# Kernel tuning notes

Hardware: AMD Instinct MI355X
Metric: run time of the kernel (lower is better)

The kernel has to match this reference:

```python
import jax, jax.numpy as jnp
import numpy as np

D_MODEL = 1024
N_HEADS = 16
FEATURE_DIM = 16
HEAD_DIM = D_MODEL // N_HEADS  # 64
EPS = 1e-12


def taylor_exp(x):
    """2nd-order Taylor feature map of exp(q^T k / sqrt(d)).
    x: (b, h, l, d) -> (b, h, l, 1 + d + d^2)"""
    d = x.shape[-1]
    rd = jnp.sqrt(jnp.asarray(d, x.dtype))      # sqrt(d)
    rrd = jnp.sqrt(rd)                          # d^(1/4)
    r2 = jnp.sqrt(jnp.asarray(2.0, x.dtype))
    x2 = (x[..., :, None] * x[..., None, :]).reshape(*x.shape[:-1], d * d) / r2
    ones = jnp.ones_like(x[..., :1])
    return jnp.concatenate([ones, x / rrd, x2 / rd], axis=-1)


def setup_inputs() -> dict:
    key = jax.random.key(0)
    k0, k1, k2, k3, k4 = jax.random.split(key, 5)
    b, l = 1, 1024
    scale = 1.0 / np.sqrt(D_MODEL)
    hidden_states = jax.random.normal(k0, (b, l, D_MODEL), dtype=jnp.float32)
    Wq = jax.random.normal(k1, (N_HEADS * FEATURE_DIM, D_MODEL), dtype=jnp.float32) * scale
    Wk = jax.random.normal(k2, (N_HEADS * FEATURE_DIM, D_MODEL), dtype=jnp.float32) * scale
    Wv = jax.random.normal(k3, (N_HEADS * HEAD_DIM, D_MODEL), dtype=jnp.float32) * scale
    Wo = jax.random.normal(k4, (D_MODEL, N_HEADS * HEAD_DIM), dtype=jnp.float32) * scale
    return {"hidden_states": hidden_states, "Wq": Wq, "Wk": Wk, "Wv": Wv, "Wo": Wo}


def reference(hidden_states, Wq, Wk, Wv, Wo):
    b, l, _ = hidden_states.shape
    # projections (bias-free)
    q = (hidden_states @ Wq.T).reshape(b, l, N_HEADS, FEATURE_DIM).transpose(0, 2, 1, 3)
    k = (hidden_states @ Wk.T).reshape(b, l, N_HEADS, FEATURE_DIM).transpose(0, 2, 1, 3)
    v = (hidden_states @ Wv.T).reshape(b, l, N_HEADS, HEAD_DIM).transpose(0, 2, 1, 3)
    qf = taylor_exp(q)   # (b, h, l, D) with D = 1 + d + d^2 = 273
    kf = taylor_exp(k)
    # causal linear attention via associative KV accumulation
    # kv_state[l] = sum_{t<=l} phi(k_t) outer v_t  -> (b, h, l, head_dim, D)
    kv_state = jnp.cumsum(kf[..., None, :] * v[..., :, None], axis=2)
    num = jnp.einsum('bhlD,bhldD->bhld', qf, kv_state)
    den = jnp.einsum('bhlD,bhlD->bhl', qf, jnp.cumsum(kf, axis=2))[..., None] + EPS
    y = num / den                                # (b, h, l, head_dim)
    y = y.transpose(0, 2, 1, 3).reshape(b, l, N_HEADS * HEAD_DIM)
    return y @ Wo.T
```

## Files before the change

### kernel.cpp

```cpp
#include <hip/hip_runtime.h>

#define LSEQ 1024
#define DMODEL 1024
#define NHEADS 16
#define FDIM 16
#define HDIM 64
#define CHUNK 64
#define NCHUNK 16
#define NSPLIT 4

typedef __attribute__((ext_vector_type(8))) short short8;
typedef __attribute__((ext_vector_type(4))) float floatx4;

__device__ __forceinline__ unsigned short f2bf(float f) {
    return __builtin_bit_cast(unsigned short, (__bf16)f);
}

__device__ __forceinline__ int block_detect_fp32(const unsigned short* wq) {
    __shared__ int cnt;
    if (threadIdx.x == 0) cnt = 0;
    __syncthreads();
    int bad = 0;
    for (int i = threadIdx.x; i < 1024; i += blockDim.x) {
        int e = (wq[i] >> 7) & 0xFF;
        if (e >= 143 || (e > 0 && e <= 80)) bad++;
    }
    if (bad) atomicAdd(&cnt, bad);
    __syncthreads();
    return cnt > 128;
}

#define U_QB   0
#define U_KB   262144
#define U_VT   524288
#define U_YB   1572864
#define U_END  2621440

#define MFMA(a, b, c) __builtin_amdgcn_mfma_f32_16x16x32_bf16((a), (b), (c), 0, 0, 0)

__device__ __forceinline__ void gemm64_body(
    unsigned short (&As)[64][136], unsigned short (&Bs)[64][136],
    const void* Araw, int a_fp32, int arow0,
    const void* Braw, int b_fp32, int brow0, floatx4 acc[4]) {
    int t = threadIdx.x;
    int r = t >> 2, c0 = (t & 3) * 32;
    int wave = t >> 6, lane = t & 63;
    int ml = lane & 15, q4 = lane >> 4;
    int mq = (wave >> 1) * 32, nq = (wave & 1) * 32;
    #pragma unroll
    for (int i = 0; i < 4; ++i) acc[i] = (floatx4){0.f, 0.f, 0.f, 0.f};

    short8 av[4], bv[4], av2[4], bv2[4];
    auto cvt8 = [](float4 f0, float4 f1) {
        short8 x;
        x[0] = (short)f2bf(f0.x); x[1] = (short)f2bf(f0.y);
        x[2] = (short)f2bf(f0.z); x[3] = (short)f2bf(f0.w);
        x[4] = (short)f2bf(f1.x); x[5] = (short)f2bf(f1.y);
        x[6] = (short)f2bf(f1.z); x[7] = (short)f2bf(f1.w);
        return x;
    };
    auto stage = [&](int k0, short8* a, short8* b) {
        if (!a_fp32) {
            const unsigned short* Ap = (const unsigned short*)Araw + (size_t)(arow0 + r) * DMODEL + k0 + c0;
            #pragma unroll
            for (int j = 0; j < 4; ++j) a[j] = *(const short8*)(Ap + j * 8);
        } else {
            const float* Ap = (const float*)Araw + (size_t)(arow0 + r) * DMODEL + k0 + c0;
            #pragma unroll
            for (int j = 0; j < 4; ++j)
                a[j] = cvt8(*(const float4*)(Ap + j * 8), *(const float4*)(Ap + j * 8 + 4));
        }
        if (!b_fp32) {
            const unsigned short* Bp = (const unsigned short*)Braw + (size_t)(brow0 + r) * DMODEL + k0 + c0;
            #pragma unroll
            for (int j = 0; j < 4; ++j) b[j] = *(const short8*)(Bp + j * 8);
        } else {
            const float* Bp = (const float*)Braw + (size_t)(brow0 + r) * DMODEL + k0 + c0;
            #pragma unroll
            for (int j = 0; j < 4; ++j)
                b[j] = cvt8(*(const float4*)(Bp + j * 8), *(const float4*)(Bp + j * 8 + 4));
        }
    };

    stage(0, av, bv);
    for (int k0 = 0; k0 < DMODEL; k0 += 128) {
        __syncthreads();
        #pragma unroll
        for (int j = 0; j < 4; ++j) {
            *(short8*)&As[r][c0 + j * 8] = av[j];
            *(short8*)&Bs[r][c0 + j * 8] = bv[j];
        }
        __syncthreads();
        if (k0 + 128 < DMODEL) stage(k0 + 128, av2, bv2);
        #pragma unroll
        for (int kk = 0; kk < 4; ++kk) {
            short8 a0 = *(const short8*)&As[mq + ml][kk * 32 + q4 * 8];
            short8 a1 = *(const short8*)&As[mq + 16 + ml][kk * 32 + q4 * 8];
            short8 b0 = *(const short8*)&Bs[nq + ml][kk * 32 + q4 * 8];
            short8 b1 = *(const short8*)&Bs[nq + 16 + ml][kk * 32 + q4 * 8];
            acc[0] = MFMA(a0, b0, acc[0]); acc[1] = MFMA(a0, b1, acc[1]);
            acc[2] = MFMA(a1, b0, acc[2]); acc[3] = MFMA(a1, b1, acc[3]);
        }
        #pragma unroll
        for (int j = 0; j < 4; ++j) { av[j] = av2[j]; bv[j] = bv2[j]; }
    }
}

__global__ __launch_bounds__(256) void qkv_gemm(
    const void* __restrict__ hidR, const void* __restrict__ WqR,
    const void* __restrict__ WkR, const void* __restrict__ WvR,
    unsigned short* __restrict__ qb, unsigned short* __restrict__ kb,
    unsigned short* __restrict__ vt) {
    int fp32 = block_detect_fp32((const unsigned short*)WqR);
    __shared__ __align__(16) unsigned short As[64][136];
    __shared__ __align__(16) unsigned short Bs[64][136];
    int nb = blockIdx.x, mb = blockIdx.y;
    const void* Braw; unsigned short* Cout; int ldc, col0, br0, isv;
    if (nb < 4)      { Braw = WqR; br0 = nb * 64;       Cout = qb; ldc = 256;  col0 = nb * 64;       isv = 0; }
    else if (nb < 8) { Braw = WkR; br0 = (nb - 4) * 64; Cout = kb; ldc = 256;  col0 = (nb - 4) * 64; isv = 0; }
    else             { Braw = WvR; br0 = (nb - 8) * 64; Cout = vt; ldc = 0;    col0 = (nb - 8) * 64; isv = 1; }

    floatx4 acc[4];
    gemm64_body(As, Bs, hidR, fp32, mb * 64, Braw, fp32, br0, acc);

    int wave = threadIdx.x >> 6, lane = threadIdx.x & 63;
    int ml = lane & 15, q4 = lane >> 4;
    int mq = (wave >> 1) * 32, nq = (wave & 1) * 32;
    if (!isv) {
        #pragma unroll
        for (int mi = 0; mi < 2; ++mi)
            #pragma unroll
            for (int ni = 0; ni < 2; ++ni) {
                floatx4 a = acc[mi * 2 + ni];
                int nloc = nq + ni * 16 + ml;
                #pragma unroll
                for (int r4 = 0; r4 < 4; ++r4) {
                    int row = mb * 64 + mq + mi * 16 + q4 * 4 + r4;
                    Cout[(size_t)row * ldc + col0 + nloc] = f2bf(a[r4]);
                }
            }
    } else {
        #pragma unroll
        for (int mi = 0; mi < 2; ++mi)
            #pragma unroll
            for (int ni = 0; ni < 2; ++ni) {
                floatx4 a = acc[mi * 2 + ni];
                int n = col0 + nq + ni * 16 + ml;
                int row0 = mb * 64 + mq + mi * 16 + q4 * 4;
                ushort4 o;
                o.x = f2bf(a[0]); o.y = f2bf(a[1]);
                o.z = f2bf(a[2]); o.w = f2bf(a[3]);
                *(ushort4*)&vt[(size_t)n * 1024 + row0] = o;
            }
    }
}

__global__ __launch_bounds__(256) void flash_partial(
    const unsigned short* __restrict__ qb, const unsigned short* __restrict__ kb,
    const unsigned short* __restrict__ vt,
    float* __restrict__ numW, float* __restrict__ denW) {
    int idx = blockIdx.x & 255;
    int s = blockIdx.x >> 8;
    int h = idx & 15, c = idx >> 4;
    int n = c + 1;
    int j0 = (n * s) >> 2;
    int j1 = ((n * (s + 1)) >> 2) - 1;
    int l0 = c * CHUNK;
    __shared__ __align__(16) unsigned short qs[64][40];
    __shared__ __align__(16) unsigned short ksm[64][40];
    __shared__ __align__(16) unsigned short vT[80][72];
    __shared__ __align__(16) unsigned short P[64][72];
    int t = threadIdx.x, lane = t & 63, wave = t >> 6;
    int ml = lane & 15, q4 = lane >> 4;
    int m0 = wave * 16;
    int sm = t >> 2, si4 = (t & 3) * 4, sc16 = (t & 3) * 16;

    {
        *(ushort4*)&qs[sm][si4] = *(const ushort4*)&qb[(size_t)(l0 + sm) * 256 + h * 16 + si4];
        ushort4 z = {0, 0, 0, 0};
        *(ushort4*)&qs[sm][16 + si4]  = z;
        *(ushort4*)&ksm[sm][16 + si4] = z;
    }
    if (t < 64) {
        vT[64][t] = 0x3F80;
        #pragma unroll
        for (int i = 65; i < 80; ++i) vT[i][t] = 0;
    }

    auto load_kv = [&](int j, ushort4& kr, short8& v0, short8& v1) {
        kr = *(const ushort4*)&kb[(size_t)(j * 64 + sm) * 256 + h * 16 + si4];
        const unsigned short* vp = vt + (size_t)(h * 64 + sm) * 1024 + j * 64 + sc16;
        v0 = *(const short8*)vp;
        v1 = *(const short8*)(vp + 8);
    };

    floatx4 acc[5];
    #pragma unroll
    for (int i = 0; i < 5; ++i) acc[i] = (floatx4){0.f, 0.f, 0.f, 0.f};

    ushort4 kr, kr2; short8 va, vb2, va2, vb22;
    if (j0 <= j1) {
        load_kv(j0, kr, va, vb2);
        for (int j = j0; j <= j1; ++j) {
            *(ushort4*)&ksm[sm][si4] = kr;
            *(short8*)&vT[sm][sc16]     = va;
            *(short8*)&vT[sm][sc16 + 8] = vb2;
            __syncthreads();
            if (j < j1) load_kv(j + 1, kr2, va2, vb22);

            short8 aq = *(const short8*)&qs[m0 + ml][q4 * 8];
            bool diag = (j == c);
            int qloc = m0 + ml;
            #pragma unroll
            for (int nt = 0; nt < 4; ++nt) {
                short8 bk = *(const short8*)&ksm[nt * 16 + ml][q4 * 8];
                floatx4 s4 = {0.f, 0.f, 0.f, 0.f};
                s4 = MFMA(bk, aq, s4);
                ushort4 pw;
                #pragma unroll
                for (int r = 0; r < 4; ++r) {
                    int tloc = nt * 16 + q4 * 4 + r;
                    float sc = s4[r];
                    float p = 1.f + 0.25f * sc + 0.03125f * sc * sc;
                    if (diag && tloc > qloc) p = 0.f;
                    ((unsigned short*)&pw)[r] = f2bf(p);
                }
                *(ushort4*)&P[qloc][nt * 16 + q4 * 4] = pw;
            }

            #pragma unroll
            for (int k0 = 0; k0 < 64; k0 += 32) {
                short8 ap = *(const short8*)&P[m0 + ml][k0 + q4 * 8];
                #pragma unroll
                for (int nt = 0; nt < 5; ++nt) {
                    short8 av = *(const short8*)&vT[nt * 16 + ml][k0 + q4 * 8];
                    acc[nt] = MFMA(av, ap, acc[nt]);
                }
            }
            __syncthreads();
            kr = kr2; va = va2; vb2 = vb22;
        }
    }

    float* np = numW + ((size_t)idx * NSPLIT + s) * 4096 + (m0 + ml) * 64;
    #pragma unroll
    for (int nt = 0; nt < 4; ++nt)
        *(floatx4*)&np[nt * 16 + q4 * 4] = acc[nt];
    if (lane < 16) denW[((size_t)idx * NSPLIT + s) * 64 + m0 + lane] = acc[4][0];
}

__global__ __launch_bounds__(256) void attn_combine(
    const float* __restrict__ numW, const float* __restrict__ denW,
    unsigned short* __restrict__ ybB) {
    int idx = blockIdx.x;
    int h = idx & 15, c = idx >> 4;
    int l0 = c * CHUNK;
    int t = threadIdx.x;
    int row = t >> 2, col0 = (t & 3) * 16;
    const float* nb_ = numW + (size_t)idx * NSPLIT * 4096 + row * 64 + col0;
    const float* db_ = denW + (size_t)idx * NSPLIT * 64 + row;
    float den = db_[0] + db_[64] + db_[128] + db_[192] + 1e-12f;
    float dinv = 1.f / den;
    float sum[16];
    #pragma unroll
    for (int u = 0; u < 16; u += 4) {
        float4 a0 = *(const float4*)(nb_ + u);
        float4 a1 = *(const float4*)(nb_ + 4096 + u);
        float4 a2 = *(const float4*)(nb_ + 8192 + u);
        float4 a3 = *(const float4*)(nb_ + 12288 + u);
        sum[u + 0] = a0.x + a1.x + a2.x + a3.x;
        sum[u + 1] = a0.y + a1.y + a2.y + a3.y;
        sum[u + 2] = a0.z + a1.z + a2.z + a3.z;
        sum[u + 3] = a0.w + a1.w + a2.w + a3.w;
    }
    short8 o0, o1;
    #pragma unroll
    for (int u = 0; u < 8; ++u)  o0[u] = (short)f2bf(sum[u] * dinv);
    #pragma unroll
    for (int u = 0; u < 8; ++u)  o1[u] = (short)f2bf(sum[u + 8] * dinv);
    unsigned short* yp = ybB + (size_t)(l0 + row) * 1024 + h * 64 + col0;
    *(short8*)yp       = o0;
    *(short8*)(yp + 8) = o1;
}

__global__ __launch_bounds__(256) void out_gemm(
    const unsigned short* __restrict__ A, const void* __restrict__ WoR,
    void* __restrict__ outv, const unsigned short* __restrict__ wqraw) {
    int fp32 = block_detect_fp32(wqraw);
    __shared__ __align__(16) unsigned short As[64][136];
    __shared__ __align__(16) unsigned short Bs[64][136];
    int nb = blockIdx.x, mb = blockIdx.y;

    floatx4 acc[4];
    gemm64_body(As, Bs, A, 0, mb * 64, WoR, fp32, nb * 64, acc);

    int wave = threadIdx.x >> 6, lane = threadIdx.x & 63;
    int ml = lane & 15, q4 = lane >> 4;
    int mq = (wave >> 1) * 32, nq = (wave & 1) * 32;
    #pragma unroll
    for (int mi = 0; mi < 2; ++mi)
        #pragma unroll
        for (int ni = 0; ni < 2; ++ni) {
            floatx4 a = acc[mi * 2 + ni];
            int nn = nb * 64 + nq + ni * 16 + ml;
            #pragma unroll
            for (int r4 = 0; r4 < 4; ++r4) {
                int row = mb * 64 + mq + mi * 16 + q4 * 4 + r4;
                size_t oidx = (size_t)row * 1024 + nn;
                if (fp32) ((float*)outv)[oidx] = a[r4];
                else      ((unsigned short*)outv)[oidx] = f2bf(a[r4]);
            }
        }
}

extern "C" void kernel_launch(void* const* d_in, const int* in_sizes, int n_in,
                              void* d_out, int out_size, void* d_ws, size_t ws_size,
                              hipStream_t stream) {
    unsigned short* us = (unsigned short*)d_ws;
    unsigned short* qbB = us + U_QB;
    unsigned short* kbB = us + U_KB;
    unsigned short* vtB = us + U_VT;
    unsigned short* ybB = us + U_YB;
    float* fws  = (float*)(us + U_END);
    float* numW = fws;
    float* denW = fws + 4194304;
    size_t need = (size_t)U_END * 2ull + (size_t)(4194304 + 65536) * 4ull;
    if (ws_size < need) return;

    qkv_gemm<<<dim3(24, 16), 256, 0, stream>>>(d_in[0], d_in[1], d_in[2], d_in[3], qbB, kbB, vtB);
    flash_partial<<<dim3(1024), 256, 0, stream>>>(qbB, kbB, vtB, numW, denW);
    attn_combine<<<dim3(256), 256, 0, stream>>>(numW, denW, ybB);
    out_gemm<<<dim3(16, 16), 256, 0, stream>>>(ybB, d_in[4], d_out, (const unsigned short*)d_in[1]);
}
```

Measured before the change: 137.6 us.

## Split K across two half-blocks in projection GEMMs with shared-memory reduction

The QKV and output projection GEMM kernels now launch 512 threads per block instead of 256. Each 256-thread half computes the same 64x64 tile over its own half of the K dimension using separate shared-memory staging buffers. The two partial accumulators are then summed through shared memory, reusing the first A buffer, before one half writes the result. This doubles the waves working on each tile, so the grids of 384 and 256 blocks keep more waves resident per CU and hide more load latency. The cost is a larger shared-memory footprint per block, an extra reduction step with its barriers, and half the threads sitting idle during the epilogue.

```diff
diff --git a/kernel.cpp b/kernel.cpp
--- a/kernel.cpp
+++ b/kernel.cpp
@@ -39,12 +39,12 @@
 #define MFMA(a, b, c) __builtin_amdgcn_mfma_f32_16x16x32_bf16((a), (b), (c), 0, 0, 0)
 
 __device__ __forceinline__ void gemm64_body(
-    unsigned short (&As)[64][136], unsigned short (&Bs)[64][136],
+    int t, unsigned short (*As)[136], unsigned short (*Bs)[136],
     const void* Araw, int a_fp32, int arow0,
-    const void* Braw, int b_fp32, int brow0, floatx4 acc[4]) {
-    int t = threadIdx.x;
+    const void* Braw, int b_fp32, int brow0,
+    int kbeg, int kend, floatx4 acc[4]) {
     int r = t >> 2, c0 = (t & 3) * 32;
-    int wave = t >> 6, lane = t & 63;
+    int wave = (t >> 6) & 3, lane = t & 63;
     int ml = lane & 15, q4 = lane >> 4;
     int mq = (wave >> 1) * 32, nq = (wave & 1) * 32;
     #pragma unroll
@@ -82,8 +82,8 @@
         }
     };
 
-    stage(0, av, bv);
-    for (int k0 = 0; k0 < DMODEL; k0 += 128) {
+    stage(kbeg, av, bv);
+    for (int k0 = kbeg; k0 < kend; k0 += 128) {
         __syncthreads();
         #pragma unroll
         for (int j = 0; j < 4; ++j) {
@@ -91,7 +91,7 @@
             *(short8*)&Bs[r][c0 + j * 8] = bv[j];
         }
         __syncthreads();
-        if (k0 + 128 < DMODEL) stage(k0 + 128, av2, bv2);
+        if (k0 + 128 < kend) stage(k0 + 128, av2, bv2);
         #pragma unroll
         for (int kk = 0; kk < 4; ++kk) {
             short8 a0 = *(const short8*)&As[mq + ml][kk * 32 + q4 * 8];
@@ -106,14 +106,40 @@
     }
 }
 
-__global__ __launch_bounds__(256) void qkv_gemm(
+__device__ __forceinline__ bool splitk_reduce(
+    int t, int hf, float* red, floatx4 acc[4]) {
+    int wave = (t >> 6) & 3, lane = t & 63;
+    int ml = lane & 15, q4 = lane >> 4;
+    int mq = (wave >> 1) * 32, nq = (wave & 1) * 32;
+    __syncthreads();
+    if (hf) {
+        #pragma unroll
+        for (int mi = 0; mi < 2; ++mi)
+            #pragma unroll
+            for (int ni = 0; ni < 2; ++ni)
+                *(floatx4*)&red[(nq + ni * 16 + ml) * 68 + mq + mi * 16 + q4 * 4] = acc[mi * 2 + ni];
+    }
+    __syncthreads();
+    if (hf) return false;
+    #pragma unroll
+    for (int mi = 0; mi < 2; ++mi)
+        #pragma unroll
+        for (int ni = 0; ni < 2; ++ni) {
+            floatx4 o = *(const floatx4*)&red[(nq + ni * 16 + ml) * 68 + mq + mi * 16 + q4 * 4];
+            acc[mi * 2 + ni] = acc[mi * 2 + ni] + o;
+        }
+    return true;
+}
+
+__global__ __launch_bounds__(512) void qkv_gemm(
     const void* __restrict__ hidR, const void* __restrict__ WqR,
     const void* __restrict__ WkR, const void* __restrict__ WvR,
     unsigned short* __restrict__ qb, unsigned short* __restrict__ kb,
     unsigned short* __restrict__ vt) {
     int fp32 = block_detect_fp32((const unsigned short*)WqR);
-    __shared__ __align__(16) unsigned short As[64][136];
-    __shared__ __align__(16) unsigned short Bs[64][136];
+    __shared__ __align__(16) unsigned short As0[64][136], Bs0[64][136];
+    __shared__ __align__(16) unsigned short As1[64][136], Bs1[64][136];
+    int t = threadIdx.x & 255, hf = threadIdx.x >> 8;
     int nb = blockIdx.x, mb = blockIdx.y;
     const void* Braw; unsigned short* Cout; int ldc, col0, br0, isv;
     if (nb < 4)      { Braw = WqR; br0 = nb * 64;       Cout = qb; ldc = 256;  col0 = nb * 64;       isv = 0; }
@@ -121,9 +147,12 @@
     else             { Braw = WvR; br0 = (nb - 8) * 64; Cout = vt; ldc = 0;    col0 = (nb - 8) * 64; isv = 1; }
 
     floatx4 acc[4];
-    gemm64_body(As, Bs, hidR, fp32, mb * 64, Braw, fp32, br0, acc);
-
-    int wave = threadIdx.x >> 6, lane = threadIdx.x & 63;
+    gemm64_body(t, hf ? As1 : As0, hf ? Bs1 : Bs0,
+                hidR, fp32, mb * 64, Braw, fp32, br0,
+                hf * 512, hf * 512 + 512, acc);
+    if (!splitk_reduce(t, hf, (float*)As0, acc)) return;
+
+    int wave = (t >> 6) & 3, lane = t & 63;
     int ml = lane & 15, q4 = lane >> 4;
     int mq = (wave >> 1) * 32, nq = (wave & 1) * 32;
     if (!isv) {
@@ -283,18 +312,22 @@
     *(short8*)(yp + 8) = o1;
 }
 
-__global__ __launch_bounds__(256) void out_gemm(
+__global__ __launch_bounds__(512) void out_gemm(
     const unsigned short* __restrict__ A, const void* __restrict__ WoR,
     void* __restrict__ outv, const unsigned short* __restrict__ wqraw) {
     int fp32 = block_detect_fp32(wqraw);
-    __shared__ __align__(16) unsigned short As[64][136];
-    __shared__ __align__(16) unsigned short Bs[64][136];
+    __shared__ __align__(16) unsigned short As0[64][136], Bs0[64][136];
+    __shared__ __align__(16) unsigned short As1[64][136], Bs1[64][136];
+    int t = threadIdx.x & 255, hf = threadIdx.x >> 8;
     int nb = blockIdx.x, mb = blockIdx.y;
 
     floatx4 acc[4];
-    gemm64_body(As, Bs, A, 0, mb * 64, WoR, fp32, nb * 64, acc);
-
-    int wave = threadIdx.x >> 6, lane = threadIdx.x & 63;
+    gemm64_body(t, hf ? As1 : As0, hf ? Bs1 : Bs0,
+                A, 0, mb * 64, WoR, fp32, nb * 64,
+                hf * 512, hf * 512 + 512, acc);
+    if (!splitk_reduce(t, hf, (float*)As0, acc)) return;
+
+    int wave = (t >> 6) & 3, lane = t & 63;
     int ml = lane & 15, q4 = lane >> 4;
     int mq = (wave >> 1) * 32, nq = (wave & 1) * 32;
     #pragma unroll
@@ -327,8 +360,8 @@
     size_t need = (size_t)U_END * 2ull + (size_t)(4194304 + 65536) * 4ull;
     if (ws_size < need) return;
 
-    qkv_gemm<<<dim3(24, 16), 256, 0, stream>>>(d_in[0], d_in[1], d_in[2], d_in[3], qbB, kbB, vtB);
+    qkv_gemm<<<dim3(24, 16), 512, 0, stream>>>(d_in[0], d_in[1], d_in[2], d_in[3], qbB, kbB, vtB);
     flash_partial<<<dim3(1024), 256, 0, stream>>>(qbB, kbB, vtB, numW, denW);
     attn_combine<<<dim3(256), 256, 0, stream>>>(numW, denW, ybB);
-    out_gemm<<<dim3(16, 16), 256, 0, stream>>>(ybB, d_in[4], d_out, (const unsigned short*)d_in[1]);
-}
+    out_gemm<<<dim3(16, 16), 512, 0, stream>>>(ybB, d_in[4], d_out, (const unsigned short*)d_in[1]);
+}
```

Result: no change. 136.1 us (-1.1%).

## Fuse all four stages into one cooperative persistent kernel with grid syncs

Applied to the files above, without the earlier changes.

Replaces the four separate launches (QKV GEMM, flash partial, combine, output GEMM) with a single cooperative kernel of 512 blocks that runs each stage in turn, separated by grid.sync(). Each block handles two flash units, pairing bid with 1023-bid so heavy and light causal chunks share a block, and reuses one shared-memory buffer across stages. The aim is to remove kernel launch gaps and inter-kernel drain. In exchange, the QKV stage now runs on only 384 of the 512 blocks and the combine and output stages on 256, there are three grid-wide barriers, and occupancy is capped by launch_bounds(256,2).

```diff
diff --git a/kernel.cpp b/kernel.cpp
--- a/kernel.cpp
+++ b/kernel.cpp
@@ -1,4 +1,7 @@
 #include <hip/hip_runtime.h>
+#include <hip/hip_cooperative_groups.h>
+
+namespace cg = cooperative_groups;
 
 #define LSEQ 1024
 #define DMODEL 1024
@@ -16,35 +19,34 @@
     return __builtin_bit_cast(unsigned short, (__bf16)f);
 }
 
-__device__ __forceinline__ int block_detect_fp32(const unsigned short* wq) {
-    __shared__ int cnt;
-    if (threadIdx.x == 0) cnt = 0;
+#define U_QB   0
+#define U_KB   262144
+#define U_VT   524288
+#define U_YB   1572864
+#define U_END  2621440
+
+#define MFMA(a, b, c) __builtin_amdgcn_mfma_f32_16x16x32_bf16((a), (b), (c), 0, 0, 0)
+
+__device__ __forceinline__ int block_detect_fp32(const unsigned short* wq, int* cnt) {
+    if (threadIdx.x == 0) *cnt = 0;
     __syncthreads();
     int bad = 0;
     for (int i = threadIdx.x; i < 1024; i += blockDim.x) {
         int e = (wq[i] >> 7) & 0xFF;
         if (e >= 143 || (e > 0 && e <= 80)) bad++;
     }
-    if (bad) atomicAdd(&cnt, bad);
+    if (bad) atomicAdd(cnt, bad);
     __syncthreads();
-    return cnt > 128;
-}
-
-#define U_QB   0
-#define U_KB   262144
-#define U_VT   524288
-#define U_YB   1572864
-#define U_END  2621440
-
-#define MFMA(a, b, c) __builtin_amdgcn_mfma_f32_16x16x32_bf16((a), (b), (c), 0, 0, 0)
+    return *cnt > 128;
+}
 
 __device__ __forceinline__ void gemm64_body(
-    unsigned short (&As)[64][136], unsigned short (&Bs)[64][136],
+    int t, unsigned short (*As)[136], unsigned short (*Bs)[136],
     const void* Araw, int a_fp32, int arow0,
-    const void* Braw, int b_fp32, int brow0, floatx4 acc[4]) {
-    int t = threadIdx.x;
+    const void* Braw, int b_fp32, int brow0,
+    int kbeg, int kend, floatx4 acc[4]) {
     int r = t >> 2, c0 = (t & 3) * 32;
-    int wave = t >> 6, lane = t & 63;
+    int wave = (t >> 6) & 3, lane = t & 63;
     int ml = lane & 15, q4 = lane >> 4;
     int mq = (wave >> 1) * 32, nq = (wave & 1) * 32;
     #pragma unroll
@@ -82,8 +84,8 @@
         }
     };
 
-    stage(0, av, bv);
-    for (int k0 = 0; k0 < DMODEL; k0 += 128) {
+    stage(kbeg, av, bv);
+    for (int k0 = kbeg; k0 < kend; k0 += 128) {
         __syncthreads();
         #pragma unroll
         for (int j = 0; j < 4; ++j) {
@@ -91,7 +93,7 @@
             *(short8*)&Bs[r][c0 + j * 8] = bv[j];
         }
         __syncthreads();
-        if (k0 + 128 < DMODEL) stage(k0 + 128, av2, bv2);
+        if (k0 + 128 < kend) stage(k0 + 128, av2, bv2);
         #pragma unroll
         for (int kk = 0; kk < 4; ++kk) {
             short8 a0 = *(const short8*)&As[mq + ml][kk * 32 + q4 * 8];
@@ -106,70 +108,20 @@
     }
 }
 
-__global__ __launch_bounds__(256) void qkv_gemm(
-    const void* __restrict__ hidR, const void* __restrict__ WqR,
-    const void* __restrict__ WkR, const void* __restrict__ WvR,
-    unsigned short* __restrict__ qb, unsigned short* __restrict__ kb,
-    unsigned short* __restrict__ vt) {
-    int fp32 = block_detect_fp32((const unsigned short*)WqR);
-    __shared__ __align__(16) unsigned short As[64][136];
-    __shared__ __align__(16) unsigned short Bs[64][136];
-    int nb = blockIdx.x, mb = blockIdx.y;
-    const void* Braw; unsigned short* Cout; int ldc, col0, br0, isv;
-    if (nb < 4)      { Braw = WqR; br0 = nb * 64;       Cout = qb; ldc = 256;  col0 = nb * 64;       isv = 0; }
-    else if (nb < 8) { Braw = WkR; br0 = (nb - 4) * 64; Cout = kb; ldc = 256;  col0 = (nb - 4) * 64; isv = 0; }
-    else             { Braw = WvR; br0 = (nb - 8) * 64; Cout = vt; ldc = 0;    col0 = (nb - 8) * 64; isv = 1; }
-
-    floatx4 acc[4];
-    gemm64_body(As, Bs, hidR, fp32, mb * 64, Braw, fp32, br0, acc);
-
-    int wave = threadIdx.x >> 6, lane = threadIdx.x & 63;
-    int ml = lane & 15, q4 = lane >> 4;
-    int mq = (wave >> 1) * 32, nq = (wave & 1) * 32;
-    if (!isv) {
-        #pragma unroll
-        for (int mi = 0; mi < 2; ++mi)
-            #pragma unroll
-            for (int ni = 0; ni < 2; ++ni) {
-                floatx4 a = acc[mi * 2 + ni];
-                int nloc = nq + ni * 16 + ml;
-                #pragma unroll
-                for (int r4 = 0; r4 < 4; ++r4) {
-                    int row = mb * 64 + mq + mi * 16 + q4 * 4 + r4;
-                    Cout[(size_t)row * ldc + col0 + nloc] = f2bf(a[r4]);
-                }
-            }
-    } else {
-        #pragma unroll
-        for (int mi = 0; mi < 2; ++mi)
-            #pragma unroll
-            for (int ni = 0; ni < 2; ++ni) {
-                floatx4 a = acc[mi * 2 + ni];
-                int n = col0 + nq + ni * 16 + ml;
-                int row0 = mb * 64 + mq + mi * 16 + q4 * 4;
-                ushort4 o;
-                o.x = f2bf(a[0]); o.y = f2bf(a[1]);
-                o.z = f2bf(a[2]); o.w = f2bf(a[3]);
-                *(ushort4*)&vt[(size_t)n * 1024 + row0] = o;
-            }
-    }
-}
-
-__global__ __launch_bounds__(256) void flash_partial(
+__device__ __forceinline__ void flash_unit(
+    int u,
+    unsigned short (*qs)[40], unsigned short (*ksm)[40],
+    unsigned short (*vT)[72], unsigned short (*P)[72],
     const unsigned short* __restrict__ qb, const unsigned short* __restrict__ kb,
     const unsigned short* __restrict__ vt,
     float* __restrict__ numW, float* __restrict__ denW) {
-    int idx = blockIdx.x & 255;
-    int s = blockIdx.x >> 8;
+    int idx = u & 255;
+    int s = u >> 8;
     int h = idx & 15, c = idx >> 4;
     int n = c + 1;
     int j0 = (n * s) >> 2;
     int j1 = ((n * (s + 1)) >> 2) - 1;
     int l0 = c * CHUNK;
-    __shared__ __align__(16) unsigned short qs[64][40];
-    __shared__ __align__(16) unsigned short ksm[64][40];
-    __shared__ __align__(16) unsigned short vT[80][72];
-    __shared__ __align__(16) unsigned short P[64][72];
     int t = threadIdx.x, lane = t & 63, wave = t >> 6;
     int ml = lane & 15, q4 = lane >> 4;
     int m0 = wave * 16;
@@ -249,68 +201,132 @@
     if (lane < 16) denW[((size_t)idx * NSPLIT + s) * 64 + m0 + lane] = acc[4][0];
 }
 
-__global__ __launch_bounds__(256) void attn_combine(
-    const float* __restrict__ numW, const float* __restrict__ denW,
-    unsigned short* __restrict__ ybB) {
-    int idx = blockIdx.x;
-    int h = idx & 15, c = idx >> 4;
-    int l0 = c * CHUNK;
-    int t = threadIdx.x;
-    int row = t >> 2, col0 = (t & 3) * 16;
-    const float* nb_ = numW + (size_t)idx * NSPLIT * 4096 + row * 64 + col0;
-    const float* db_ = denW + (size_t)idx * NSPLIT * 64 + row;
-    float den = db_[0] + db_[64] + db_[128] + db_[192] + 1e-12f;
-    float dinv = 1.f / den;
-    float sum[16];
-    #pragma unroll
-    for (int u = 0; u < 16; u += 4) {
-        float4 a0 = *(const float4*)(nb_ + u);
-        float4 a1 = *(const float4*)(nb_ + 4096 + u);
-        float4 a2 = *(const float4*)(nb_ + 8192 + u);
-        float4 a3 = *(const float4*)(nb_ + 12288 + u);
-        sum[u + 0] = a0.x + a1.x + a2.x + a3.x;
-        sum[u + 1] = a0.y + a1.y + a2.y + a3.y;
-        sum[u + 2] = a0.z + a1.z + a2.z + a3.z;
-        sum[u + 3] = a0.w + a1.w + a2.w + a3.w;
-    }
-    short8 o0, o1;
-    #pragma unroll
-    for (int u = 0; u < 8; ++u)  o0[u] = (short)f2bf(sum[u] * dinv);
-    #pragma unroll
-    for (int u = 0; u < 8; ++u)  o1[u] = (short)f2bf(sum[u + 8] * dinv);
-    unsigned short* yp = ybB + (size_t)(l0 + row) * 1024 + h * 64 + col0;
-    *(short8*)yp       = o0;
-    *(short8*)(yp + 8) = o1;
-}
-
-__global__ __launch_bounds__(256) void out_gemm(
-    const unsigned short* __restrict__ A, const void* __restrict__ WoR,
-    void* __restrict__ outv, const unsigned short* __restrict__ wqraw) {
-    int fp32 = block_detect_fp32(wqraw);
-    __shared__ __align__(16) unsigned short As[64][136];
-    __shared__ __align__(16) unsigned short Bs[64][136];
-    int nb = blockIdx.x, mb = blockIdx.y;
-
-    floatx4 acc[4];
-    gemm64_body(As, Bs, A, 0, mb * 64, WoR, fp32, nb * 64, acc);
-
-    int wave = threadIdx.x >> 6, lane = threadIdx.x & 63;
-    int ml = lane & 15, q4 = lane >> 4;
-    int mq = (wave >> 1) * 32, nq = (wave & 1) * 32;
-    #pragma unroll
-    for (int mi = 0; mi < 2; ++mi)
-        #pragma unroll
-        for (int ni = 0; ni < 2; ++ni) {
-            floatx4 a = acc[mi * 2 + ni];
-            int nn = nb * 64 + nq + ni * 16 + ml;
-            #pragma unroll
-            for (int r4 = 0; r4 < 4; ++r4) {
-                int row = mb * 64 + mq + mi * 16 + q4 * 4 + r4;
-                size_t oidx = (size_t)row * 1024 + nn;
-                if (fp32) ((float*)outv)[oidx] = a[r4];
-                else      ((unsigned short*)outv)[oidx] = f2bf(a[r4]);
+__global__ __launch_bounds__(256, 2) void fused_all(
+    const void* __restrict__ hidR, const void* __restrict__ WqR,
+    const void* __restrict__ WkR, const void* __restrict__ WvR,
+    const void* __restrict__ WoR, void* __restrict__ outv,
+    unsigned short* __restrict__ qb, unsigned short* __restrict__ kb,
+    unsigned short* __restrict__ vt, unsigned short* __restrict__ yb,
+    float* __restrict__ numW, float* __restrict__ denW) {
+    cg::grid_group grid = cg::this_grid();
+    __shared__ __align__(16) unsigned char smem[34816];
+    __shared__ int cnt_sh;
+    int bid = blockIdx.x, t = threadIdx.x;
+    int fp32 = block_detect_fp32((const unsigned short*)WqR, &cnt_sh);
+
+    if (bid < 384) {
+        unsigned short (*As)[136] = (unsigned short(*)[136])smem;
+        unsigned short (*Bs)[136] = (unsigned short(*)[136])(smem + 17408);
+        int nb = bid % 24, mb = bid / 24;
+        const void* Braw; unsigned short* Cout; int ldc, col0, br0, isv;
+        if (nb < 4)      { Braw = WqR; br0 = nb * 64;       Cout = qb; ldc = 256;  col0 = nb * 64;       isv = 0; }
+        else if (nb < 8) { Braw = WkR; br0 = (nb - 4) * 64; Cout = kb; ldc = 256;  col0 = (nb - 4) * 64; isv = 0; }
+        else             { Braw = WvR; br0 = (nb - 8) * 64; Cout = vt; ldc = 0;    col0 = (nb - 8) * 64; isv = 1; }
+
+        floatx4 acc[4];
+        gemm64_body(t, As, Bs, hidR, fp32, mb * 64, Braw, fp32, br0, 0, DMODEL, acc);
+
+        int wave = (t >> 6) & 3, lane = t & 63;
+        int ml = lane & 15, q4 = lane >> 4;
+        int mq = (wave >> 1) * 32, nq = (wave & 1) * 32;
+        if (!isv) {
+            #pragma unroll
+            for (int mi = 0; mi < 2; ++mi)
+                #pragma unroll
+                for (int ni = 0; ni < 2; ++ni) {
+                    floatx4 a = acc[mi * 2 + ni];
+                    int nloc = nq + ni * 16 + ml;
+                    #pragma unroll
+                    for (int r4 = 0; r4 < 4; ++r4) {
+                        int row = mb * 64 + mq + mi * 16 + q4 * 4 + r4;
+                        Cout[(size_t)row * ldc + col0 + nloc] = f2bf(a[r4]);
+                    }
+                }
+        } else {
+            #pragma unroll
+            for (int mi = 0; mi < 2; ++mi)
+                #pragma unroll
+                for (int ni = 0; ni < 2; ++ni) {
+                    floatx4 a = acc[mi * 2 + ni];
+                    int nn = col0 + nq + ni * 16 + ml;
+                    int row0 = mb * 64 + mq + mi * 16 + q4 * 4;
+                    ushort4 o;
+                    o.x = f2bf(a[0]); o.y = f2bf(a[1]);
+                    o.z = f2bf(a[2]); o.w = f2bf(a[3]);
+                    *(ushort4*)&vt[(size_t)nn * 1024 + row0] = o;
+                }
+        }
+    }
+    grid.sync();
+
+    {
+        unsigned short (*qs)[40]  = (unsigned short(*)[40])smem;
+        unsigned short (*ksm)[40] = (unsigned short(*)[40])(smem + 5120);
+        unsigned short (*vT)[72]  = (unsigned short(*)[72])(smem + 10240);
+        unsigned short (*P)[72]   = (unsigned short(*)[72])(smem + 21760);
+        flash_unit(bid,        qs, ksm, vT, P, qb, kb, vt, numW, denW);
+        flash_unit(1023 - bid, qs, ksm, vT, P, qb, kb, vt, numW, denW);
+    }
+    grid.sync();
+
+    if (bid < 256) {
+        int idx = bid;
+        int h = idx & 15, c = idx >> 4;
+        int l0 = c * CHUNK;
+        int row = t >> 2, col0 = (t & 3) * 16;
+        const float* nb_ = numW + (size_t)idx * NSPLIT * 4096 + row * 64 + col0;
+        const float* db_ = denW + (size_t)idx * NSPLIT * 64 + row;
+        float den = db_[0] + db_[64] + db_[128] + db_[192] + 1e-12f;
+        float dinv = 1.f / den;
+        float sum[16];
+        #pragma unroll
+        for (int u = 0; u < 16; u += 4) {
+            float4 a0 = *(const float4*)(nb_ + u);
+            float4 a1 = *(const float4*)(nb_ + 4096 + u);
+            float4 a2 = *(const float4*)(nb_ + 8192 + u);
+            float4 a3 = *(const float4*)(nb_ + 12288 + u);
+            sum[u + 0] = a0.x + a1.x + a2.x + a3.x;
+            sum[u + 1] = a0.y + a1.y + a2.y + a3.y;
+            sum[u + 2] = a0.z + a1.z + a2.z + a3.z;
+            sum[u + 3] = a0.w + a1.w + a2.w + a3.w;
+        }
+        short8 o0, o1;
+        #pragma unroll
+        for (int u = 0; u < 8; ++u)  o0[u] = (short)f2bf(sum[u] * dinv);
+        #pragma unroll
+        for (int u = 0; u < 8; ++u)  o1[u] = (short)f2bf(sum[u + 8] * dinv);
+        unsigned short* yp = yb + (size_t)(l0 + row) * 1024 + h * 64 + col0;
+        *(short8*)yp       = o0;
+        *(short8*)(yp + 8) = o1;
+    }
+    grid.sync();
+
+    if (bid < 256) {
+        unsigned short (*As)[136] = (unsigned short(*)[136])smem;
+        unsigned short (*Bs)[136] = (unsigned short(*)[136])(smem + 17408);
+        int nb = bid & 15, mb = bid >> 4;
+
+        floatx4 acc[4];
+        gemm64_body(t, As, Bs, yb, 0, mb * 64, WoR, fp32, nb * 64, 0, DMODEL, acc);
+
+        int wave = (t >> 6) & 3, lane = t & 63;
+        int ml = lane & 15, q4 = lane >> 4;
+        int mq = (wave >> 1) * 32, nq = (wave & 1) * 32;
+        #pragma unroll
+        for (int mi = 0; mi < 2; ++mi)
+            #pragma unroll
+            for (int ni = 0; ni < 2; ++ni) {
+                floatx4 a = acc[mi * 2 + ni];
+                int nn = nb * 64 + nq + ni * 16 + ml;
+                #pragma unroll
+                for (int r4 = 0; r4 < 4; ++r4) {
+                    int row = mb * 64 + mq + mi * 16 + q4 * 4 + r4;
+                    size_t oidx = (size_t)row * 1024 + nn;
+                    if (fp32) ((float*)outv)[oidx] = a[r4];
+                    else      ((unsigned short*)outv)[oidx] = f2bf(a[r4]);
+                }
             }
-        }
+    }
 }
 
 extern "C" void kernel_launch(void* const* d_in, const int* in_sizes, int n_in,
@@ -327,8 +343,10 @@
     size_t need = (size_t)U_END * 2ull + (size_t)(4194304 + 65536) * 4ull;
     if (ws_size < need) return;
 
-    qkv_gemm<<<dim3(24, 16), 256, 0, stream>>>(d_in[0], d_in[1], d_in[2], d_in[3], qbB, kbB, vtB);
-    flash_partial<<<dim3(1024), 256, 0, stream>>>(qbB, kbB, vtB, numW, denW);
-    attn_combine<<<dim3(256), 256, 0, stream>>>(numW, denW, ybB);
-    out_gemm<<<dim3(16, 16), 256, 0, stream>>>(ybB, d_in[4], d_out, (const unsigned short*)d_in[1]);
-}
+    void* hidR = d_in[0]; void* WqR = d_in[1]; void* WkR = d_in[2];
+    void* WvR = d_in[3];  void* WoR = d_in[4]; void* outv = d_out;
+    void* args[] = { &hidR, &WqR, &WkR, &WvR, &WoR, &outv,
+                     &qbB, &kbB, &vtB, &ybB, &numW, &denW };
+    hipLaunchCooperativeKernel((const void*)fused_all, dim3(512), dim3(256),
+                               args, 0, stream);
+}
```

Result: slower. 332.7 us (+141.8%).
